# Performance work log

Hardware: AMD Instinct MI355X
Metric: run time of the kernel (lower is better)

Reference implementation:

```python
import jax, jax.numpy as jnp
import numpy as np

EPS_LN = 1e-5

def layer_norm(x, g, b):
    mu = x.mean(-1, keepdims=True)
    var = ((x - mu) ** 2).mean(-1, keepdims=True)
    return (x - mu) / jnp.sqrt(var + EPS_LN) * g + b

def spike(x):
    # MultiSpike: quantized spike activation, forward = clip(round(x), 0, 4)
    return jnp.clip(jnp.round(x), 0.0, 4.0)

def setup_inputs() -> dict:
    key = jax.random.key(0)
    ks = jax.random.split(key, 8)
    B, C, H, W = 16, 256, 56, 56
    hid = 128
    inp = {}
    inp['feature_map'] = jax.random.normal(ks[0], (B, C, H, W), jnp.float32)
    inp['audio_feature'] = jax.random.normal(ks[1], (B, 1, C), jnp.float32)
    # MINE params
    inp['w1'] = jax.random.normal(ks[2], (hid, 2 * C), jnp.float32) / np.sqrt(2 * C)
    inp['b1'] = jnp.zeros((hid,), jnp.float32)
    inp['g1'] = jnp.ones((hid,), jnp.float32)
    inp['beta1'] = jnp.zeros((hid,), jnp.float32)
    inp['w2'] = jax.random.normal(ks[3], (hid // 2, hid), jnp.float32) / np.sqrt(hid)
    inp['b2'] = jnp.zeros((hid // 2,), jnp.float32)
    inp['g2'] = jnp.ones((hid // 2,), jnp.float32)
    inp['beta2'] = jnp.zeros((hid // 2,), jnp.float32)
    inp['w3'] = jax.random.normal(ks[4], (1, hid // 2), jnp.float32) / np.sqrt(hid // 2)
    inp['b3'] = jnp.zeros((1,), jnp.float32)
    # MI params
    inp['pw'] = jax.random.normal(ks[5], (C, C), jnp.float32) / np.sqrt(C)
    inp['pb'] = jnp.zeros((C,), jnp.float32)
    inp['pg'] = jnp.ones((C,), jnp.float32)
    inp['pbeta'] = jnp.zeros((C,), jnp.float32)
    return inp

def reference(feature_map, audio_feature, w1, b1, g1, beta1, w2, b2, g2, beta2,
              w3, b3, pw, pb, pg, pbeta):
    B, C, H, W = feature_map.shape
    # visual tokens: [B*H*W, C]
    visual = feature_map.transpose(0, 2, 3, 1).reshape(B * H * W, C)
    # broadcast audio to every spatial position: [B*H*W, C]
    audio = jnp.broadcast_to(audio_feature[:, 0][:, None, None, :], (B, H, W, C)).reshape(B * H * W, C)
    # MINE MLP on joint features
    joint = jnp.concatenate([visual, audio], axis=1)            # [BHW, 2C]
    h = spike(layer_norm(joint @ w1.T + b1, g1, beta1))          # [BHW, 128]
    h = spike(layer_norm(h @ w2.T + b2, g2, beta2))              # [BHW, 64]
    mi = (h @ w3.T + b3)[:, 0]                                   # [BHW]
    mi_map = mi.reshape(B, 1, H * W)
    fm_flat = feature_map.reshape(B, C, H * W)
    # MI-weighted pooling: [B,1,C]
    x = jnp.einsum('bos,bcs->boc', mi_map, fm_flat)
    x = x @ pw.T + pb                                            # proj (dropout = eval identity)
    x = spike(layer_norm(x, pg, pbeta))                          # [B,1,C]
    fusion_map = jnp.einsum('bchw,bc->bchw', feature_map, x[:, 0])
    mi4 = mi_map.reshape(B, 1, H, W)
    mi4 = (mi4 - mi4.min()) / (mi4.max() - mi4.min() + 1e-6)     # global min-max norm
    return fusion_map, mi4
```

## Files before the change

### kernel.cpp

```cpp
#include <hip/hip_runtime.h>

#define HW 3136
#define NPOS 12845056

__device__ __forceinline__ unsigned fkey(float f) {
  unsigned u = __float_as_uint(f);
  return (u & 0x80000000u) ? ~u : (u | 0x80000000u);
}
__device__ __forceinline__ float funkey(unsigned u) {
  return __uint_as_float((u & 0x80000000u) ? (u & 0x7FFFFFFFu) : ~u);
}
__device__ __forceinline__ float spikef(float x) {
  return fminf(fmaxf(rintf(x), 0.0f), 4.0f);
}

__global__ __launch_bounds__(256) void prep_kernel(
    const float* __restrict__ audio, const float* __restrict__ w1,
    const float* __restrict__ b1, const float* __restrict__ w2,
    float* __restrict__ a_pre, float* __restrict__ w1t,
    float* __restrict__ w2t, float* __restrict__ pool,
    unsigned* __restrict__ mm)
{
  __shared__ float au[256];
  const int bx = blockIdx.x, t = threadIdx.x;
  if (bx < 128) {
    int idx = bx * 256 + t;
    int c = idx >> 7, j = idx & 127;
    w1t[idx] = w1[j * 512 + c];
  } else if (bx < 160) {
    int idx = (bx - 128) * 256 + t;
    int k = idx >> 6, j2 = idx & 63;
    w2t[idx] = w2[j2 * 128 + k];
  } else if (bx < 176) {
    int b = bx - 160;
    au[t] = audio[b * 256 + t];
    __syncthreads();
    int w = t >> 6, l = t & 63;
    float a0 = au[l], a1 = au[l + 64], a2 = au[l + 128], a3 = au[l + 192];
    for (int jj = 0; jj < 32; ++jj) {
      int j = w * 32 + jj;
      const float* row = w1 + j * 512 + 256;
      float s = row[l] * a0 + row[l + 64] * a1 + row[l + 128] * a2 + row[l + 192] * a3;
      #pragma unroll
      for (int off = 32; off; off >>= 1) s += __shfl_xor(s, off);
      if (l == 0) a_pre[b * 128 + j] = s + b1[j];
    }
  } else {
    for (int i = t; i < 4096; i += 256) pool[i] = 0.0f;
    if (t == 0) { mm[0] = 0xFFFFFFFFu; mm[1] = 0u; }
  }
}

__global__ __launch_bounds__(256, 2) void mlp_kernel(
    const float* __restrict__ fm, const float* __restrict__ w1t,
    const float* __restrict__ w2t, const float* __restrict__ b2,
    const float* __restrict__ w3, const float* __restrict__ b3,
    const float* __restrict__ g1, const float* __restrict__ be1,
    const float* __restrict__ g2, const float* __restrict__ be2,
    const float* __restrict__ a_pre, float* __restrict__ mi_out,
    float* __restrict__ pool, unsigned* __restrict__ mm)
{
  __shared__ unsigned pk[32 * 128];
  __shared__ float red1[4][128];
  __shared__ float red2[4][128];
  __shared__ float miL[128];

  const int b  = blockIdx.y;
  const int s0 = blockIdx.x * 128;
  const int t  = threadIdx.x;
  const int l  = t & 63;
  const int w  = __builtin_amdgcn_readfirstlane(t >> 6);
  const bool has2 = (s0 + 128) <= HW;
  const size_t off2 = has2 ? 64 : 0;

  const float* fmp = fm + (size_t)b * 256 * HW + s0 + l;

  float acc0[32], acc1[32];
  #pragma unroll
  for (int j = 0; j < 32; ++j) { acc0[j] = 0.f; acc1[j] = 0.f; }

  const float* wq = w1t + w * 32;

  float xa0[8], xa1[8], xb0[8], xb1[8];
  #pragma unroll
  for (int i = 0; i < 8; ++i) {
    size_t o = (size_t)i * HW;
    xa0[i] = fmp[o]; xa1[i] = fmp[o + off2];
  }

  auto stage = [&](int cbase, float (&c0)[8], float (&c1)[8],
                   float (&n0)[8], float (&n1)[8], bool pre) {
    if (pre) {
      #pragma unroll
      for (int i = 0; i < 8; ++i) {
        size_t o = (size_t)(cbase + 8 + i) * HW;
        n0[i] = fmp[o]; n1[i] = fmp[o + off2];
      }
    }
    #pragma unroll
    for (int cl = 0; cl < 8; ++cl) {
      const float* wr = wq + (cbase + cl) * 128;
      float x0 = c0[cl], x1 = c1[cl];
      #pragma unroll
      for (int j = 0; j < 32; ++j) {
        acc0[j] = fmaf(x0, wr[j], acc0[j]);
        acc1[j] = fmaf(x1, wr[j], acc1[j]);
      }
    }
  };
  #pragma unroll 1
  for (int sp = 0; sp < 16; ++sp) {
    stage(sp * 16,     xa0, xa1, xb0, xb1, true);
    stage(sp * 16 + 8, xb0, xb1, xa0, xa1, sp < 15);
  }
  {
    const float* ap = a_pre + b * 128 + w * 32;
    #pragma unroll
    for (int j = 0; j < 32; ++j) { acc0[j] += ap[j]; acc1[j] += ap[j]; }
  }

  {
    float s0s = 0.f, s1s = 0.f;
    #pragma unroll
    for (int j = 0; j < 32; ++j) { s0s += acc0[j]; s1s += acc1[j]; }
    red1[w][l] = s0s; red1[w][64 + l] = s1s;
  }
  __syncthreads();
  float mu0 = (red1[0][l] + red1[1][l] + red1[2][l] + red1[3][l]) * (1.0f / 128.0f);
  float mu1 = (red1[0][64+l] + red1[1][64+l] + red1[2][64+l] + red1[3][64+l]) * (1.0f / 128.0f);
  {
    float v0 = 0.f, v1 = 0.f;
    #pragma unroll
    for (int j = 0; j < 32; ++j) {
      float d0 = acc0[j] - mu0; v0 = fmaf(d0, d0, v0);
      float d1 = acc1[j] - mu1; v1 = fmaf(d1, d1, v1);
    }
    red2[w][l] = v0; red2[w][64 + l] = v1;
  }
  __syncthreads();
  float var0 = (red2[0][l] + red2[1][l] + red2[2][l] + red2[3][l]) * (1.0f / 128.0f);
  float var1 = (red2[0][64+l] + red2[1][64+l] + red2[2][64+l] + red2[3][64+l]) * (1.0f / 128.0f);
  float inv0 = 1.0f / sqrtf(var0 + 1e-5f);
  float inv1 = 1.0f / sqrtf(var1 + 1e-5f);
  {
    const float* g1q  = g1  + w * 32;
    const float* be1q = be1 + w * 32;
    #pragma unroll
    for (int q = 0; q < 8; ++q) {
      unsigned u0 = 0, u1 = 0;
      #pragma unroll
      for (int bb = 0; bb < 4; ++bb) {
        int j = q * 4 + bb;
        float gv = g1q[j], bv = be1q[j];
        float v0 = spikef((acc0[j] - mu0) * inv0 * gv + bv);
        float v1 = spikef((acc1[j] - mu1) * inv1 * gv + bv);
        u0 |= ((unsigned)v0) << (8 * bb);
        u1 |= ((unsigned)v1) << (8 * bb);
      }
      pk[(w * 8 + q) * 128 + l]      = u0;
      pk[(w * 8 + q) * 128 + 64 + l] = u1;
    }
  }
  __syncthreads();

  float a20[16], a21[16];
  #pragma unroll
  for (int j = 0; j < 16; ++j) { a20[j] = 0.f; a21[j] = 0.f; }
  const float* w2q = w2t + w * 16;
  #pragma unroll 2
  for (int kg = 0; kg < 32; ++kg) {
    unsigned u0 = pk[kg * 128 + l];
    unsigned u1 = pk[kg * 128 + 64 + l];
    #pragma unroll
    for (int kk = 0; kk < 4; ++kk) {
      const float* wr = w2q + (kg * 4 + kk) * 64;
      float h0 = (float)((u0 >> (8 * kk)) & 255u);
      float h1 = (float)((u1 >> (8 * kk)) & 255u);
      #pragma unroll
      for (int j = 0; j < 16; ++j) {
        a20[j] = fmaf(h0, wr[j], a20[j]);
        a21[j] = fmaf(h1, wr[j], a21[j]);
      }
    }
  }

  float h20[16], h21[16];
  {
    const float* b2q = b2 + w * 16;
    float sm0 = 0.f, sm1 = 0.f;
    #pragma unroll
    for (int j = 0; j < 16; ++j) {
      h20[j] = a20[j] + b2q[j]; sm0 += h20[j];
      h21[j] = a21[j] + b2q[j]; sm1 += h21[j];
    }
    red1[w][l] = sm0; red1[w][64 + l] = sm1;
  }
  __syncthreads();
  float mu20 = (red1[0][l] + red1[1][l] + red1[2][l] + red1[3][l]) * (1.0f / 64.0f);
  float mu21 = (red1[0][64+l] + red1[1][64+l] + red1[2][64+l] + red1[3][64+l]) * (1.0f / 64.0f);
  {
    float v0 = 0.f, v1 = 0.f;
    #pragma unroll
    for (int j = 0; j < 16; ++j) {
      float d0 = h20[j] - mu20; v0 = fmaf(d0, d0, v0);
      float d1 = h21[j] - mu21; v1 = fmaf(d1, d1, v1);
    }
    red2[w][l] = v0; red2[w][64 + l] = v1;
  }
  __syncthreads();
  float var20 = (red2[0][l] + red2[1][l] + red2[2][l] + red2[3][l]) * (1.0f / 64.0f);
  float var21 = (red2[0][64+l] + red2[1][64+l] + red2[2][64+l] + red2[3][64+l]) * (1.0f / 64.0f);
  float inv20 = 1.0f / sqrtf(var20 + 1e-5f);
  float inv21 = 1.0f / sqrtf(var21 + 1e-5f);
  float mip0 = 0.f, mip1 = 0.f;
  {
    const float* g2q  = g2  + w * 16;
    const float* be2q = be2 + w * 16;
    const float* w3q  = w3  + w * 16;
    #pragma unroll
    for (int j = 0; j < 16; ++j) {
      float gv = g2q[j], bv = be2q[j], wv = w3q[j];
      float p0 = spikef((h20[j] - mu20) * inv20 * gv + bv);
      float p1 = spikef((h21[j] - mu21) * inv21 * gv + bv);
      mip0 = fmaf(p0, wv, mip0);
      mip1 = fmaf(p1, wv, mip1);
    }
  }
  red1[w][l] = mip0; red1[w][64 + l] = mip1;
  __syncthreads();
  if (w == 0) {
    float mi0 = red1[0][l] + red1[1][l] + red1[2][l] + red1[3][l] + b3[0];
    float mi1 = red1[0][64+l] + red1[1][64+l] + red1[2][64+l] + red1[3][64+l] + b3[0];
    mi_out[b * HW + s0 + l] = mi0;
    if (has2) mi_out[b * HW + s0 + 64 + l] = mi1;
    miL[l] = mi0;
    miL[64 + l] = has2 ? mi1 : 0.0f;
    float mn = has2 ? fminf(mi0, mi1) : mi0;
    float mx = has2 ? fmaxf(mi0, mi1) : mi0;
    #pragma unroll
    for (int off = 32; off; off >>= 1) {
      mn = fminf(mn, __shfl_xor(mn, off));
      mx = fmaxf(mx, __shfl_xor(mx, off));
    }
    if (l == 0) {
      unsigned kmn = fkey(mn), kmx = fkey(mx);
      volatile unsigned* vmm = (volatile unsigned*)mm;
      if (kmn < vmm[0]) atomicMin(&mm[0], kmn);
      if (kmx > vmm[1]) atomicMax(&mm[1], kmx);
    }
  }
  __syncthreads();

  const float m0 = miL[l], m1 = miL[64 + l];
  #pragma unroll 4
  for (int ci = 0; ci < 64; ++ci) {
    int c = (w << 6) + ci;
    size_t o = (size_t)c * HW;
    float v = fmp[o] * m0 + fmp[o + off2] * m1;
    #pragma unroll
    for (int off = 32; off; off >>= 1) v += __shfl_xor(v, off);
    if (l == 0) atomicAdd(&pool[b * 256 + c], v);
  }
}

__global__ __launch_bounds__(256) void scale_kernel(
    const float* __restrict__ pool, const float* __restrict__ pw,
    const float* __restrict__ pb, const float* __restrict__ pg,
    const float* __restrict__ pbeta, float* __restrict__ scale,
    const unsigned* __restrict__ mm, float* __restrict__ gpar)
{
  __shared__ float pl[256];
  __shared__ float xsh[256];
  __shared__ float rs[4], rs2[4];
  int b = blockIdx.x, t = threadIdx.x;
  pl[t] = pool[b*256 + t];
  __syncthreads();
  int w = t >> 6, l = t & 63;
  float p0 = pl[l], p1 = pl[l+64], p2 = pl[l+128], p3 = pl[l+192];
  for (int jj = 0; jj < 64; ++jj) {
    int j = w*64 + jj;
    const float* row = pw + j*256;
    float s = row[l]*p0 + row[l+64]*p1 + row[l+128]*p2 + row[l+192]*p3;
    #pragma unroll
    for (int off = 32; off; off >>= 1) s += __shfl_xor(s, off);
    if (l == 0) xsh[j] = s;
  }
  __syncthreads();
  float x = xsh[t] + pb[t];
  float s = x;
  #pragma unroll
  for (int off = 32; off; off >>= 1) s += __shfl_xor(s, off);
  if (l == 0) rs[w] = s;
  __syncthreads();
  float mu = (rs[0]+rs[1]+rs[2]+rs[3]) * (1.0f/256.0f);
  float d = x - mu;
  float s2 = d*d;
  #pragma unroll
  for (int off = 32; off; off >>= 1) s2 += __shfl_xor(s2, off);
  if (l == 0) rs2[w] = s2;
  __syncthreads();
  float var = (rs2[0]+rs2[1]+rs2[2]+rs2[3]) * (1.0f/256.0f);
  float v = d / sqrtf(var + 1e-5f) * pg[t] + pbeta[t];
  scale[b*256 + t] = spikef(v);
  if (b == 0 && t == 0) {
    float mn = funkey(mm[0]), mx = funkey(mm[1]);
    gpar[0] = mn;
    gpar[1] = mx - mn + 1e-6f;
  }
}

__global__ __launch_bounds__(256) void fuse_kernel(
    const float4* __restrict__ fm4, const float* __restrict__ scale,
    const float4* __restrict__ mi4, const float* __restrict__ gpar,
    float4* __restrict__ out4, float4* __restrict__ mi4out)
{
  const int c = blockIdx.x, b = blockIdx.y, t = threadIdx.x;
  if (c < 256) {
    float s = scale[b * 256 + c];
    size_t base = ((size_t)b * 256 + c) * 784;
    #pragma unroll
    for (int i = 0; i < 3; ++i) {
      int idx = t + i * 256;
      float4 v = fm4[base + idx];
      out4[base + idx] = make_float4(v.x*s, v.y*s, v.z*s, v.w*s);
    }
    int idx = t + 768;
    if (idx < 784) {
      float4 v = fm4[base + idx];
      out4[base + idx] = make_float4(v.x*s, v.y*s, v.z*s, v.w*s);
    }
  } else {
    float gmin = gpar[0], den = gpar[1];
    size_t base = (size_t)b * 784;
    #pragma unroll
    for (int i = 0; i < 3; ++i) {
      int idx = t + i * 256;
      float4 v = mi4[base + idx];
      mi4out[base + idx] = make_float4((v.x-gmin)/den, (v.y-gmin)/den,
                                       (v.z-gmin)/den, (v.w-gmin)/den);
    }
    int idx = t + 768;
    if (idx < 784) {
      float4 v = mi4[base + idx];
      mi4out[base + idx] = make_float4((v.x-gmin)/den, (v.y-gmin)/den,
                                       (v.z-gmin)/den, (v.w-gmin)/den);
    }
  }
}

extern "C" void kernel_launch(void* const* d_in, const int* in_sizes, int n_in,
                              void* d_out, int out_size, void* d_ws, size_t ws_size,
                              hipStream_t stream)
{
  const float* fm    = (const float*)d_in[0];
  const float* audio = (const float*)d_in[1];
  const float* w1    = (const float*)d_in[2];
  const float* b1    = (const float*)d_in[3];
  const float* g1    = (const float*)d_in[4];
  const float* be1   = (const float*)d_in[5];
  const float* w2    = (const float*)d_in[6];
  const float* b2    = (const float*)d_in[7];
  const float* g2    = (const float*)d_in[8];
  const float* be2   = (const float*)d_in[9];
  const float* w3    = (const float*)d_in[10];
  const float* b3    = (const float*)d_in[11];
  const float* pw    = (const float*)d_in[12];
  const float* pb    = (const float*)d_in[13];
  const float* pg    = (const float*)d_in[14];
  const float* pbeta = (const float*)d_in[15];

  float* ws    = (float*)d_ws;
  float* a_pre = ws;
  float* pool  = ws + 2048;
  float* scale = ws + 6144;
  float* mi    = ws + 10240;
  float* w1t   = ws + 60416;
  float* w2t   = ws + 93184;
  unsigned* mm = (unsigned*)(ws + 101376);
  float* gpar  = ws + 101378;

  float* out    = (float*)d_out;
  float* mi4out = out + NPOS;

  prep_kernel<<<177, 256, 0, stream>>>(audio, w1, b1, w2, a_pre, w1t, w2t,
                                       pool, mm);
  mlp_kernel<<<dim3(25, 16), 256, 0, stream>>>(fm, w1t, w2t, b2, w3, b3,
                                               g1, be1, g2, be2,
                                               a_pre, mi, pool, mm);
  scale_kernel<<<16, 256, 0, stream>>>(pool, pw, pb, pg, pbeta, scale, mm, gpar);
  fuse_kernel<<<dim3(257, 16), 256, 0, stream>>>((const float4*)fm, scale,
                                                 (const float4*)mi, gpar,
                                                 (float4*)out, (float4*)mi4out);
}
```

Before: 329.8 us.

## Stream feature-map chunks into LDS via async global_load_lds double buffering

The MLP kernel used to prefetch feature-map channel values into register double buffers. It now copies 16-channel chunks straight into a double-buffered LDS array with global_load_lds DMA, and the FMA loop reads its inputs from LDS. This is meant to free the VGPRs the prefetch buffers held and overlap loads with compute. Launch bounds also rise from 2 to 4 blocks per SM to raise occupancy, which risks register spills given the 64 accumulators, and it adds a barrier per chunk.

```diff
diff --git a/kernel.cpp b/kernel.cpp
--- a/kernel.cpp
+++ b/kernel.cpp
@@ -51,7 +51,7 @@
   }
 }
 
-__global__ __launch_bounds__(256, 2) void mlp_kernel(
+__global__ __launch_bounds__(256, 4) void mlp_kernel(
     const float* __restrict__ fm, const float* __restrict__ w1t,
     const float* __restrict__ w2t, const float* __restrict__ b2,
     const float* __restrict__ w3, const float* __restrict__ b3,
@@ -60,6 +60,7 @@
     const float* __restrict__ a_pre, float* __restrict__ mi_out,
     float* __restrict__ pool, unsigned* __restrict__ mm)
 {
+  __shared__ float fmbuf[2][16 * 128];
   __shared__ unsigned pk[32 * 128];
   __shared__ float red1[4][128];
   __shared__ float red2[4][128];
@@ -73,7 +74,22 @@
   const bool has2 = (s0 + 128) <= HW;
   const size_t off2 = has2 ? 64 : 0;
 
-  const float* fmp = fm + (size_t)b * 256 * HW + s0 + l;
+  const float* fmblk = fm + (size_t)b * 256 * HW + s0;
+  const float* fmp   = fmblk + l;
+  const int pq = has2 ? ((l & 31) * 4) : ((l & 15) * 4);
+
+  auto issue_chunk = [&](int ch, int bufid) {
+    const int cbase = ch * 16;
+    #pragma unroll
+    for (int q = 0; q < 2; ++q) {
+      int cidx = cbase + q * 8 + w * 2 + (l >> 5);
+      const float* gsrc = fmblk + (size_t)cidx * HW + pq;
+      float* ldst = &fmbuf[bufid][(q * 8 + w * 2) * 128];
+      __builtin_amdgcn_global_load_lds(
+          (const __attribute__((address_space(1))) void*)gsrc,
+          (__attribute__((address_space(3))) void*)ldst, 16, 0, 0);
+    }
+  };
 
   float acc0[32], acc1[32];
   #pragma unroll
@@ -81,37 +97,24 @@
 
   const float* wq = w1t + w * 32;
 
-  float xa0[8], xa1[8], xb0[8], xb1[8];
-  #pragma unroll
-  for (int i = 0; i < 8; ++i) {
-    size_t o = (size_t)i * HW;
-    xa0[i] = fmp[o]; xa1[i] = fmp[o + off2];
-  }
-
-  auto stage = [&](int cbase, float (&c0)[8], float (&c1)[8],
-                   float (&n0)[8], float (&n1)[8], bool pre) {
-    if (pre) {
-      #pragma unroll
-      for (int i = 0; i < 8; ++i) {
-        size_t o = (size_t)(cbase + 8 + i) * HW;
-        n0[i] = fmp[o]; n1[i] = fmp[o + off2];
-      }
-    }
-    #pragma unroll
-    for (int cl = 0; cl < 8; ++cl) {
+  issue_chunk(0, 0);
+  #pragma unroll 1
+  for (int ch = 0; ch < 16; ++ch) {
+    __syncthreads();
+    if (ch < 15) issue_chunk(ch + 1, (ch + 1) & 1);
+    const float* buf = fmbuf[ch & 1];
+    const int cbase = ch * 16;
+    #pragma unroll
+    for (int cl = 0; cl < 16; ++cl) {
       const float* wr = wq + (cbase + cl) * 128;
-      float x0 = c0[cl], x1 = c1[cl];
+      float x0 = buf[cl * 128 + l];
+      float x1 = buf[cl * 128 + 64 + l];
       #pragma unroll
       for (int j = 0; j < 32; ++j) {
         acc0[j] = fmaf(x0, wr[j], acc0[j]);
         acc1[j] = fmaf(x1, wr[j], acc1[j]);
       }
     }
-  };
-  #pragma unroll 1
-  for (int sp = 0; sp < 16; ++sp) {
-    stage(sp * 16,     xa0, xa1, xb0, xb1, true);
-    stage(sp * 16 + 8, xb0, xb1, xa0, xa1, sp < 15);
   }
   {
     const float* ap = a_pre + b * 128 + w * 32;
```

Result: slower. 378.6 us (+14.8%).
